# Kernel tuning notes

Measured on AMD Instinct MI355X. Metric: run time of the kernel, lower is better.

## Reference

```python
import jax, jax.numpy as jnp
import numpy as np

B, L, D, H, FFN = 4, 1024, 1024, 16, 4096
DPH = D // H
EPS = 1e-5

def layer_norm(x, g, b):
    mu = jnp.mean(x, axis=-1, keepdims=True)
    var = jnp.mean(jnp.square(x - mu), axis=-1, keepdims=True)
    return (x - mu) * jax.lax.rsqrt(var + EPS) * g + b

def setup_inputs() -> dict:
    key = jax.random.key(0)
    ks = jax.random.split(key, 12)
    s = 0.02
    return {
        "inputs": jax.random.normal(ks[0], (B, L, D), dtype=jnp.float32),
        "Wq": jax.random.normal(ks[1], (D, D), dtype=jnp.float32) * s,
        "bq": jnp.zeros((D,), jnp.float32),
        "Wk": jax.random.normal(ks[2], (D, D), dtype=jnp.float32) * s,
        "bk": jnp.zeros((D,), jnp.float32),
        "Wv": jax.random.normal(ks[3], (D, D), dtype=jnp.float32) * s,
        "bv": jnp.zeros((D,), jnp.float32),
        "Wo": jax.random.normal(ks[4], (D, D), dtype=jnp.float32) * s,
        "bo": jnp.zeros((D,), jnp.float32),
        "ln1_g": jnp.ones((D,), jnp.float32),
        "ln1_b": jnp.zeros((D,), jnp.float32),
        "W1": jax.random.normal(ks[5], (D, FFN), dtype=jnp.float32) * s,  # conv1d k=1 == linear
        "b1": jnp.zeros((FFN,), jnp.float32),
        "W2": jax.random.normal(ks[6], (FFN, D), dtype=jnp.float32) * s,
        "b2": jnp.zeros((D,), jnp.float32),
        "ln2_g": jnp.ones((D,), jnp.float32),
        "ln2_b": jnp.zeros((D,), jnp.float32),
    }

def reference(inputs, Wq, bq, Wk, bk, Wv, bv, Wo, bo, ln1_g, ln1_b,
              W1, b1, W2, b2, ln2_g, ln2_b):
    residual = inputs
    # QKV projections, then the original's raw view(B*H, L, DPH) split (NOT a transpose split)
    q = (inputs @ Wq + bq).reshape(B * H, L, DPH)
    k = (inputs @ Wk + bk).reshape(B * H, L, DPH)
    v = (inputs @ Wv + bv).reshape(B * H, L, DPH)
    scale = DPH ** -0.5
    scores = jnp.einsum('bqd,bkd->bqk', q, k) * scale  # [B*H, L, L]
    attention = jax.nn.softmax(scores, axis=-1)
    context = jnp.einsum('bqk,bkd->bqd', attention, v).reshape(B, L, D)
    out = context @ Wo + bo
    out = layer_norm(residual + out, ln1_g, ln1_b)
    # Positionwise FFN: two 1x1 conv1d == two linears with relu
    ffn = jax.nn.relu(out @ W1 + b1) @ W2 + b2
    out = layer_norm(out + ffn, ln2_g, ln2_b)
    return out, attention
```

## Files before the change

kernel.cpp:

```cpp
#include <hip/hip_runtime.h>
#include <hip/hip_bf16.h>
#include <stdint.h>


using bf16_t  = __hip_bfloat16;
using short8  = __attribute__((ext_vector_type(8))) short;
using short4v = __attribute__((ext_vector_type(4))) short;
using f32x4   = __attribute__((ext_vector_type(4))) float;

#define DEV static __device__ __forceinline__

DEV short bfbits(float f) {
  bf16_t h = __float2bfloat16(f);
  union { bf16_t h; short s; } u; u.h = h; return u.s;
}

__global__ __launch_bounds__(256) void k_f32_to_bf16(const float* __restrict__ in,
                                                     bf16_t* __restrict__ out) {
  size_t i = ((size_t)blockIdx.x * 256 + threadIdx.x) * 4;
  f32x4 x = *(const f32x4*)(in + i);
  short4v o;
  o[0] = bfbits(x[0]); o[1] = bfbits(x[1]); o[2] = bfbits(x[2]); o[3] = bfbits(x[3]);
  *(short4v*)((short*)out + i) = o;
}

__global__ __launch_bounds__(256) void k_transpose_f32_bf16(const float* __restrict__ in,
                                                            bf16_t* __restrict__ out,
                                                            int R, int C) {
  __shared__ float tile[32][33];
  int tx = threadIdx.x & 31, ty = threadIdx.x >> 5;
  int r0 = blockIdx.y * 32, c0 = blockIdx.x * 32;
  #pragma unroll
  for (int i = 0; i < 4; ++i)
    tile[ty + i * 8][tx] = in[(size_t)(r0 + ty + i * 8) * C + c0 + tx];
  __syncthreads();
  #pragma unroll
  for (int i = 0; i < 4; ++i)
    out[(size_t)(c0 + ty + i * 8) * R + r0 + tx] = __float2bfloat16(tile[tx][ty + i * 8]);
}

__global__ __launch_bounds__(256) void k_transpose_bf16_b(const bf16_t* __restrict__ in,
                                                          bf16_t* __restrict__ out,
                                                          int R, int C, long sIn, long sOut) {
  __shared__ bf16_t tile[32][33];
  const bf16_t* inz = in + (size_t)blockIdx.z * sIn;
  bf16_t* outz = out + (size_t)blockIdx.z * sOut;
  int tx = threadIdx.x & 31, ty = threadIdx.x >> 5;
  int r0 = blockIdx.y * 32, c0 = blockIdx.x * 32;
  #pragma unroll
  for (int i = 0; i < 4; ++i)
    tile[ty + i * 8][tx] = inz[(size_t)(r0 + ty + i * 8) * C + c0 + tx];
  __syncthreads();
  #pragma unroll
  for (int i = 0; i < 4; ++i)
    outz[(size_t)(c0 + ty + i * 8) * R + r0 + tx] = tile[tx][ty + i * 8];
}

template<int BM, int BN, bool AF32, bool ALPHA, bool BIAS, bool RELU, bool RESID,
         bool OUTF, bool OUTB>
__global__ __launch_bounds__(256)
void k_gemm_bt(const void* __restrict__ Ap, const bf16_t* __restrict__ Btp,
               float* __restrict__ Cf, bf16_t* __restrict__ Cb,
               const float* __restrict__ bias, const float* __restrict__ resid,
               int Kdim, int lda, int ldb, int ldc, float alpha,
               long strA, long strB, long strC) {
  constexpr int BK = 32, LDSK = 40;
  constexpr int WTM = BM / 2, WTN = BN / 2;
  constexpr int MI = WTM / 16, NI = WTN / 16;
  __shared__ __align__(16) bf16_t sA[BM][LDSK];
  __shared__ __align__(16) bf16_t sB[BN][LDSK];

  const int tid = threadIdx.x;
  const int lane = tid & 63;
  const int wv = tid >> 6;
  const int wm = wv & 1, wn = wv >> 1;
  const int z = blockIdx.z;
  const size_t m0 = (size_t)blockIdx.y * BM;
  const size_t n0 = (size_t)blockIdx.x * BN;

  const bf16_t* A16 = AF32 ? nullptr : ((const bf16_t*)Ap + (size_t)z * strA);
  const float*  A32 = AF32 ? ((const float*)Ap + (size_t)z * strA) : nullptr;
  const bf16_t* Bp  = Btp + (size_t)z * strB;

  f32x4 acc[MI][NI] = {};

  const int srow = tid >> 2;
  const int skc  = (tid & 3) * 8;

  for (int k0 = 0; k0 < Kdim; k0 += BK) {
    #pragma unroll
    for (int j = 0; j < BM / 64; ++j) {
      int r = j * 64 + srow;
      if (AF32) {
        const float* p = A32 + (m0 + r) * (size_t)lda + k0 + skc;
        f32x4 f0 = *(const f32x4*)p;
        f32x4 f1 = *(const f32x4*)(p + 4);
        short8 v;
        v[0] = bfbits(f0[0]); v[1] = bfbits(f0[1]); v[2] = bfbits(f0[2]); v[3] = bfbits(f0[3]);
        v[4] = bfbits(f1[0]); v[5] = bfbits(f1[1]); v[6] = bfbits(f1[2]); v[7] = bfbits(f1[3]);
        *(short8*)(&sA[r][skc]) = v;
      } else {
        *(short8*)(&sA[r][skc]) =
            *(const short8*)(A16 + (m0 + r) * (size_t)lda + k0 + skc);
      }
    }
    #pragma unroll
    for (int j = 0; j < BN / 64; ++j) {
      int r = j * 64 + srow;
      *(short8*)(&sB[r][skc]) =
          *(const short8*)(Bp + (n0 + r) * (size_t)ldb + k0 + skc);
    }
    __syncthreads();

    const int fm = wm * WTM + (lane & 15);
    const int fn = wn * WTN + (lane & 15);
    const int fk = (lane >> 4) * 8;
    short8 av[MI], bvv[NI];
    #pragma unroll
    for (int mi = 0; mi < MI; ++mi) av[mi] = *(const short8*)(&sA[fm + mi * 16][fk]);
    #pragma unroll
    for (int ni = 0; ni < NI; ++ni) bvv[ni] = *(const short8*)(&sB[fn + ni * 16][fk]);
    #pragma unroll
    for (int mi = 0; mi < MI; ++mi)
      #pragma unroll
      for (int ni = 0; ni < NI; ++ni)
        acc[mi][ni] = __builtin_amdgcn_mfma_f32_16x16x32_bf16(av[mi], bvv[ni],
                                                              acc[mi][ni], 0, 0, 0);
    __syncthreads();
  }

  const size_t cz = (size_t)z * strC;
  const int col0 = (int)n0 + wn * WTN + (lane & 15);
  const int row0 = (int)m0 + wm * WTM + ((lane >> 4) << 2);
  #pragma unroll
  for (int ni = 0; ni < NI; ++ni) {
    const int col = col0 + ni * 16;
    const float bval = BIAS ? bias[col] : 0.0f;
    #pragma unroll
    for (int mi = 0; mi < MI; ++mi) {
      #pragma unroll
      for (int r = 0; r < 4; ++r) {
        int row = row0 + mi * 16 + r;
        float v = acc[mi][ni][r];
        if (ALPHA) v *= alpha;
        v += bval;
        size_t off = cz + (size_t)row * ldc + col;
        if (RESID) v += resid[off];
        if (RELU) v = fmaxf(v, 0.0f);
        if (OUTF) Cf[off] = v;
        if (OUTB) Cb[off] = __float2bfloat16(v);
      }
    }
  }
}

__global__ __launch_bounds__(256) void k_flash_attn(const bf16_t* __restrict__ Qb,
                                                    const bf16_t* __restrict__ Kb,
                                                    const bf16_t* __restrict__ Vt,
                                                    float* __restrict__ attn,
                                                    bf16_t* __restrict__ ctx) {
  constexpr int LP = 72;
  __shared__ __align__(16) bf16_t sQ[128][LP];
  __shared__ __align__(16) bf16_t sK[64][LP];
  __shared__ __align__(16) bf16_t sP[128][LP];
  __shared__ __align__(16) bf16_t sV[64][LP];

  const int tid = threadIdx.x;
  const int lane = tid & 63;
  const int wv = tid >> 6;
  const int z = blockIdx.y;
  const int m0 = blockIdx.x * 128;

  const bf16_t* Qz = Qb + (size_t)z * 65536;
  const bf16_t* Kz = Kb + (size_t)z * 65536;
  const bf16_t* Vz = Vt + (size_t)z * 65536;
  float* az = attn + (size_t)z * 1048576;
  bf16_t* cz = ctx + (size_t)z * 65536;

  #pragma unroll
  for (int j = 0; j < 4; ++j) {
    int ii = j * 256 + tid;
    int r = ii >> 3, c = (ii & 7) * 8;
    *(short8*)(&sQ[r][c]) = *(const short8*)(Qz + (size_t)(m0 + r) * 64 + c);
  }
  __syncthreads();

  const int fr = lane & 15;
  const int fk = (lane >> 4) * 8;
  const int crow = (lane >> 4) << 2;

  short8 qf[2][2];
  #pragma unroll
  for (int mi = 0; mi < 2; ++mi)
    #pragma unroll
    for (int ks = 0; ks < 2; ++ks)
      qf[mi][ks] = *(const short8*)(&sQ[wv * 32 + mi * 16 + fr][ks * 32 + fk]);

  float m_run[2][4], s_run[2][4];
  #pragma unroll
  for (int mi = 0; mi < 2; ++mi)
    #pragma unroll
    for (int r = 0; r < 4; ++r) { m_run[mi][r] = -1e30f; s_run[mi][r] = 0.0f; }

  for (int c0 = 0; c0 < 1024; c0 += 64) {
    #pragma unroll
    for (int j = 0; j < 2; ++j) {
      int ii = j * 256 + tid;
      int r = ii >> 3, c = (ii & 7) * 8;
      *(short8*)(&sK[r][c]) = *(const short8*)(Kz + (size_t)(c0 + r) * 64 + c);
    }
    __syncthreads();
    f32x4 acc[2][4] = {};
    #pragma unroll
    for (int ks = 0; ks < 2; ++ks) {
      short8 bf[4];
      #pragma unroll
      for (int ni = 0; ni < 4; ++ni)
        bf[ni] = *(const short8*)(&sK[ni * 16 + fr][ks * 32 + fk]);
      #pragma unroll
      for (int mi = 0; mi < 2; ++mi)
        #pragma unroll
        for (int ni = 0; ni < 4; ++ni)
          acc[mi][ni] = __builtin_amdgcn_mfma_f32_16x16x32_bf16(qf[mi][ks], bf[ni],
                                                                acc[mi][ni], 0, 0, 0);
    }
    __syncthreads();
    #pragma unroll
    for (int mi = 0; mi < 2; ++mi)
      #pragma unroll
      for (int r = 0; r < 4; ++r) {
        float mx = fmaxf(fmaxf(acc[0][0][r], acc[0][0][r]), acc[mi][0][r]);
        mx = acc[mi][0][r];
        #pragma unroll
        for (int ni = 1; ni < 4; ++ni) mx = fmaxf(mx, acc[mi][ni][r]);
        mx *= 0.125f;
        #pragma unroll
        for (int o = 1; o < 16; o <<= 1) mx = fmaxf(mx, __shfl_xor(mx, o, 64));
        float mn = fmaxf(m_run[mi][r], mx);
        float se = 0.0f;
        #pragma unroll
        for (int ni = 0; ni < 4; ++ni) se += __expf(acc[mi][ni][r] * 0.125f - mn);
        #pragma unroll
        for (int o = 1; o < 16; o <<= 1) se += __shfl_xor(se, o, 64);
        s_run[mi][r] = s_run[mi][r] * __expf(m_run[mi][r] - mn) + se;
        m_run[mi][r] = mn;
      }
  }

  float inv_s[2][4];
  #pragma unroll
  for (int mi = 0; mi < 2; ++mi)
    #pragma unroll
    for (int r = 0; r < 4; ++r) inv_s[mi][r] = 1.0f / s_run[mi][r];

  f32x4 cacc[2][4] = {};
  for (int c0 = 0; c0 < 1024; c0 += 64) {
    #pragma unroll
    for (int j = 0; j < 2; ++j) {
      int ii = j * 256 + tid;
      int r = ii >> 3, c = (ii & 7) * 8;
      *(short8*)(&sK[r][c]) = *(const short8*)(Kz + (size_t)(c0 + r) * 64 + c);
      *(short8*)(&sV[r][c]) = *(const short8*)(Vz + (size_t)r * 1024 + c0 + c);
    }
    __syncthreads();
    f32x4 acc[2][4] = {};
    #pragma unroll
    for (int ks = 0; ks < 2; ++ks) {
      short8 bf[4];
      #pragma unroll
      for (int ni = 0; ni < 4; ++ni)
        bf[ni] = *(const short8*)(&sK[ni * 16 + fr][ks * 32 + fk]);
      #pragma unroll
      for (int mi = 0; mi < 2; ++mi)
        #pragma unroll
        for (int ni = 0; ni < 4; ++ni)
          acc[mi][ni] = __builtin_amdgcn_mfma_f32_16x16x32_bf16(qf[mi][ks], bf[ni],
                                                                acc[mi][ni], 0, 0, 0);
    }
    #pragma unroll
    for (int mi = 0; mi < 2; ++mi)
      #pragma unroll
      for (int ni = 0; ni < 4; ++ni)
        #pragma unroll
        for (int r = 0; r < 4; ++r) {
          int row = wv * 32 + mi * 16 + crow + r;
          float p = __expf(acc[mi][ni][r] * 0.125f - m_run[mi][r]) * inv_s[mi][r];
          az[(size_t)(m0 + row) * 1024 + c0 + ni * 16 + fr] = p;
          sP[row][ni * 16 + fr] = __float2bfloat16(p);
        }
    __syncthreads();
    #pragma unroll
    for (int ks = 0; ks < 2; ++ks) {
      short8 pa[2], vb[4];
      #pragma unroll
      for (int mi = 0; mi < 2; ++mi)
        pa[mi] = *(const short8*)(&sP[wv * 32 + mi * 16 + fr][ks * 32 + fk]);
      #pragma unroll
      for (int ni = 0; ni < 4; ++ni)
        vb[ni] = *(const short8*)(&sV[ni * 16 + fr][ks * 32 + fk]);
      #pragma unroll
      for (int mi = 0; mi < 2; ++mi)
        #pragma unroll
        for (int ni = 0; ni < 4; ++ni)
          cacc[mi][ni] = __builtin_amdgcn_mfma_f32_16x16x32_bf16(pa[mi], vb[ni],
                                                                 cacc[mi][ni], 0, 0, 0);
    }
    __syncthreads();
  }

  #pragma unroll
  for (int mi = 0; mi < 2; ++mi)
    #pragma unroll
    for (int ni = 0; ni < 4; ++ni)
      #pragma unroll
      for (int r = 0; r < 4; ++r) {
        int row = wv * 32 + mi * 16 + crow + r;
        cz[(size_t)(m0 + row) * 64 + ni * 16 + fr] = __float2bfloat16(cacc[mi][ni][r]);
      }
}

__global__ __launch_bounds__(256) void k_layernorm(float* __restrict__ io,
                                                   bf16_t* __restrict__ ob,
                                                   const float* __restrict__ g,
                                                   const float* __restrict__ bta) {
  float* r = io + (size_t)blockIdx.x * 1024;
  const int t = threadIdx.x;
  f32x4 x = *(const f32x4*)(r + t * 4);
  float s = x[0] + x[1] + x[2] + x[3];
  float s2 = x[0] * x[0] + x[1] * x[1] + x[2] * x[2] + x[3] * x[3];
  #pragma unroll
  for (int o = 32; o > 0; o >>= 1) { s += __shfl_xor(s, o, 64); s2 += __shfl_xor(s2, o, 64); }
  __shared__ float as[4], as2[4];
  if ((t & 63) == 0) { as[t >> 6] = s; as2[t >> 6] = s2; }
  __syncthreads();
  s = as[0] + as[1] + as[2] + as[3];
  s2 = as2[0] + as2[1] + as2[2] + as2[3];
  float mu = s * (1.0f / 1024.0f);
  float var = s2 * (1.0f / 1024.0f) - mu * mu;
  float rs = rsqrtf(var + 1e-5f);
  f32x4 gg = *(const f32x4*)(g + t * 4);
  f32x4 bb = *(const f32x4*)(bta + t * 4);
  f32x4 y;
  #pragma unroll
  for (int i = 0; i < 4; ++i) y[i] = (x[i] - mu) * rs * gg[i] + bb[i];
  *(f32x4*)(r + t * 4) = y;
  if (ob) {
    short4v o4;
    o4[0] = bfbits(y[0]); o4[1] = bfbits(y[1]); o4[2] = bfbits(y[2]); o4[3] = bfbits(y[3]);
    *(short4v*)((short*)ob + (size_t)blockIdx.x * 1024 + t * 4) = o4;
  }
}

extern "C" void kernel_launch(void* const* d_in, const int* in_sizes, int n_in,
                              void* d_out, int out_size, void* d_ws, size_t ws_size,
                              hipStream_t stream) {
  (void)in_sizes; (void)n_in; (void)out_size;
  const float* inputs = (const float*)d_in[0];
  const float* Wq = (const float*)d_in[1];  const float* bq = (const float*)d_in[2];
  const float* Wk = (const float*)d_in[3];  const float* bk = (const float*)d_in[4];
  const float* Wv = (const float*)d_in[5];  const float* bv = (const float*)d_in[6];
  const float* Wo = (const float*)d_in[7];  const float* bo = (const float*)d_in[8];
  const float* ln1g = (const float*)d_in[9];  const float* ln1b = (const float*)d_in[10];
  const float* W1 = (const float*)d_in[11]; const float* b1 = (const float*)d_in[12];
  const float* W2 = (const float*)d_in[13]; const float* b2 = (const float*)d_in[14];
  const float* ln2g = (const float*)d_in[15]; const float* ln2b = (const float*)d_in[16];

  const size_t MB = 1ull << 20;
  if (ws_size < 96 * MB) return;

  char* ws = (char*)d_ws;
  bf16_t* WQT  = (bf16_t*)(ws + 0 * MB);
  bf16_t* WKT  = (bf16_t*)(ws + 2 * MB);
  bf16_t* WVT  = (bf16_t*)(ws + 4 * MB);
  bf16_t* WOT  = (bf16_t*)(ws + 6 * MB);
  bf16_t* W1T  = (bf16_t*)(ws + 8 * MB);
  bf16_t* W2T  = (bf16_t*)(ws + 16 * MB);
  bf16_t* XB   = (bf16_t*)(ws + 24 * MB);
  bf16_t* QB   = (bf16_t*)(ws + 32 * MB);
  bf16_t* KB   = (bf16_t*)(ws + 40 * MB);
  bf16_t* VB   = (bf16_t*)(ws + 48 * MB);
  bf16_t* VT   = (bf16_t*)(ws + 56 * MB);
  bf16_t* CTX  = (bf16_t*)(ws + 24 * MB);
  float*  OUT1F = (float*)(ws + 40 * MB);
  bf16_t* OUT1B = (bf16_t*)(ws + 32 * MB);
  bf16_t* HB   = (bf16_t*)(ws + 64 * MB);

  float* outF = (float*)d_out;
  float* attn = outF + 4194304;

  k_f32_to_bf16<<<4096, 256, 0, stream>>>(inputs, XB);
  k_transpose_f32_bf16<<<dim3(32, 32), 256, 0, stream>>>(Wq, WQT, 1024, 1024);
  k_transpose_f32_bf16<<<dim3(32, 32), 256, 0, stream>>>(Wk, WKT, 1024, 1024);
  k_transpose_f32_bf16<<<dim3(32, 32), 256, 0, stream>>>(Wv, WVT, 1024, 1024);
  k_transpose_f32_bf16<<<dim3(32, 32), 256, 0, stream>>>(Wo, WOT, 1024, 1024);
  k_transpose_f32_bf16<<<dim3(128, 32), 256, 0, stream>>>(W1, W1T, 1024, 4096);
  k_transpose_f32_bf16<<<dim3(32, 128), 256, 0, stream>>>(W2, W2T, 4096, 1024);

  k_gemm_bt<128, 128, false, false, true, false, false, false, true>
      <<<dim3(8, 32, 1), 256, 0, stream>>>(XB, WQT, nullptr, QB, bq, nullptr,
                                           1024, 1024, 1024, 1024, 1.0f, 0, 0, 0);
  k_gemm_bt<128, 128, false, false, true, false, false, false, true>
      <<<dim3(8, 32, 1), 256, 0, stream>>>(XB, WKT, nullptr, KB, bk, nullptr,
                                           1024, 1024, 1024, 1024, 1.0f, 0, 0, 0);
  k_gemm_bt<128, 128, false, false, true, false, false, false, true>
      <<<dim3(8, 32, 1), 256, 0, stream>>>(XB, WVT, nullptr, VB, bv, nullptr,
                                           1024, 1024, 1024, 1024, 1.0f, 0, 0, 0);

  k_transpose_bf16_b<<<dim3(2, 32, 64), 256, 0, stream>>>(VB, VT, 1024, 64, 65536, 65536);

  k_flash_attn<<<dim3(8, 64), 256, 0, stream>>>(QB, KB, VT, attn, CTX);

  k_gemm_bt<128, 128, false, false, true, false, true, true, false>
      <<<dim3(8, 32, 1), 256, 0, stream>>>(CTX, WOT, OUT1F, nullptr, bo, inputs,
                                           1024, 1024, 1024, 1024, 1.0f, 0, 0, 0);

  k_layernorm<<<4096, 256, 0, stream>>>(OUT1F, OUT1B, ln1g, ln1b);

  k_gemm_bt<128, 128, false, false, true, true, false, false, true>
      <<<dim3(32, 32, 1), 256, 0, stream>>>(OUT1B, W1T, nullptr, HB, b1, nullptr,
                                            1024, 1024, 1024, 4096, 1.0f, 0, 0, 0);

  k_gemm_bt<128, 128, false, false, true, false, true, true, false>
      <<<dim3(8, 32, 1), 256, 0, stream>>>(HB, W2T, outF, nullptr, b2, OUT1F,
                                           4096, 4096, 4096, 1024, 1.0f, 0, 0, 0);

  k_layernorm<<<4096, 256, 0, stream>>>(outF, nullptr, ln2g, ln2b);
}
```

Before: 762.2 us.

## Use direct global-to-LDS loads in GEMM and fuse QKV projections into one launch

The GEMM now stages A and B tiles with global_load_lds (16-byte direct-to-LDS loads), which skips the register round trip, and drops the padded LDS layout for a dense 32-wide row layout. The three Q/K/V projections run as one launch over a 3072-wide output, relying on WQT/WKT/WVT being contiguous in the workspace, and pick the bias and output buffer per 1024-column slice. The unpadded LDS layout may cause bank conflicts on the fragment reads. The change also removes a redundant max computation in attention.

After: 707.7 us. -7.2%, faster.

```diff
diff --git a/kernel.cpp b/kernel.cpp
--- a/kernel.cpp
+++ b/kernel.cpp
@@ -13,6 +13,12 @@
 DEV short bfbits(float f) {
   bf16_t h = __float2bfloat16(f);
   union { bf16_t h; short s; } u; u.h = h; return u.s;
+}
+
+DEV void gload_lds16(const bf16_t* g, bf16_t* lds) {
+  __builtin_amdgcn_global_load_lds(
+      (const __attribute__((address_space(1))) void*)g,
+      (__attribute__((address_space(3))) void*)lds, 16, 0, 0);
 }
 
 __global__ __launch_bounds__(256) void k_f32_to_bf16(const float* __restrict__ in,
@@ -56,70 +62,55 @@
     outz[(size_t)(c0 + ty + i * 8) * R + r0 + tx] = tile[tx][ty + i * 8];
 }
 
-template<int BM, int BN, bool AF32, bool ALPHA, bool BIAS, bool RELU, bool RESID,
-         bool OUTF, bool OUTB>
+template<int BM, int BN, bool ALPHA, bool BIAS, bool RELU, bool RESID,
+         bool OUTF, bool OUTB, bool QKV3>
 __global__ __launch_bounds__(256)
-void k_gemm_bt(const void* __restrict__ Ap, const bf16_t* __restrict__ Btp,
+void k_gemm_bt(const bf16_t* __restrict__ A, const bf16_t* __restrict__ Bt,
                float* __restrict__ Cf, bf16_t* __restrict__ Cb,
-               const float* __restrict__ bias, const float* __restrict__ resid,
-               int Kdim, int lda, int ldb, int ldc, float alpha,
-               long strA, long strB, long strC) {
-  constexpr int BK = 32, LDSK = 40;
+               const float* __restrict__ bias, const float* __restrict__ bias2,
+               const float* __restrict__ bias3, const float* __restrict__ resid,
+               int Kdim, int lda, int ldb, int ldc, float alpha) {
+  constexpr int BK = 32;
   constexpr int WTM = BM / 2, WTN = BN / 2;
   constexpr int MI = WTM / 16, NI = WTN / 16;
-  __shared__ __align__(16) bf16_t sA[BM][LDSK];
-  __shared__ __align__(16) bf16_t sB[BN][LDSK];
+  __shared__ __align__(16) bf16_t sA[BM * BK];
+  __shared__ __align__(16) bf16_t sB[BN * BK];
 
   const int tid = threadIdx.x;
   const int lane = tid & 63;
   const int wv = tid >> 6;
   const int wm = wv & 1, wn = wv >> 1;
-  const int z = blockIdx.z;
   const size_t m0 = (size_t)blockIdx.y * BM;
   const size_t n0 = (size_t)blockIdx.x * BN;
 
-  const bf16_t* A16 = AF32 ? nullptr : ((const bf16_t*)Ap + (size_t)z * strA);
-  const float*  A32 = AF32 ? ((const float*)Ap + (size_t)z * strA) : nullptr;
-  const bf16_t* Bp  = Btp + (size_t)z * strB;
-
   f32x4 acc[MI][NI] = {};
 
-  const int srow = tid >> 2;
-  const int skc  = (tid & 3) * 8;
+  const int rr = lane >> 2, cc = (lane & 3) * 8;
+  const bf16_t* Arow = A + (m0 + rr) * (size_t)lda + cc;
+  const bf16_t* Brow = Bt + (n0 + rr) * (size_t)ldb + cc;
+
+  const int fm = wm * WTM + (lane & 15);
+  const int fn = wn * WTN + (lane & 15);
+  const int fk = (lane >> 4) * 8;
 
   for (int k0 = 0; k0 < Kdim; k0 += BK) {
     #pragma unroll
     for (int j = 0; j < BM / 64; ++j) {
-      int r = j * 64 + srow;
-      if (AF32) {
-        const float* p = A32 + (m0 + r) * (size_t)lda + k0 + skc;
-        f32x4 f0 = *(const f32x4*)p;
-        f32x4 f1 = *(const f32x4*)(p + 4);
-        short8 v;
-        v[0] = bfbits(f0[0]); v[1] = bfbits(f0[1]); v[2] = bfbits(f0[2]); v[3] = bfbits(f0[3]);
-        v[4] = bfbits(f1[0]); v[5] = bfbits(f1[1]); v[6] = bfbits(f1[2]); v[7] = bfbits(f1[3]);
-        *(short8*)(&sA[r][skc]) = v;
-      } else {
-        *(short8*)(&sA[r][skc]) =
-            *(const short8*)(A16 + (m0 + r) * (size_t)lda + k0 + skc);
-      }
+      int c = j * 4 + wv;
+      gload_lds16(Arow + (size_t)c * 16 * lda + k0, sA + c * 512);
     }
     #pragma unroll
     for (int j = 0; j < BN / 64; ++j) {
-      int r = j * 64 + srow;
-      *(short8*)(&sB[r][skc]) =
-          *(const short8*)(Bp + (n0 + r) * (size_t)ldb + k0 + skc);
-    }
-    __syncthreads();
-
-    const int fm = wm * WTM + (lane & 15);
-    const int fn = wn * WTN + (lane & 15);
-    const int fk = (lane >> 4) * 8;
+      int c = j * 4 + wv;
+      gload_lds16(Brow + (size_t)c * 16 * ldb + k0, sB + c * 512);
+    }
+    __syncthreads();
+
     short8 av[MI], bvv[NI];
     #pragma unroll
-    for (int mi = 0; mi < MI; ++mi) av[mi] = *(const short8*)(&sA[fm + mi * 16][fk]);
-    #pragma unroll
-    for (int ni = 0; ni < NI; ++ni) bvv[ni] = *(const short8*)(&sB[fn + ni * 16][fk]);
+    for (int mi = 0; mi < MI; ++mi) av[mi] = *(const short8*)(sA + (fm + mi * 16) * BK + fk);
+    #pragma unroll
+    for (int ni = 0; ni < NI; ++ni) bvv[ni] = *(const short8*)(sB + (fn + ni * 16) * BK + fk);
     #pragma unroll
     for (int mi = 0; mi < MI; ++mi)
       #pragma unroll
@@ -129,13 +120,17 @@
     __syncthreads();
   }
 
-  const size_t cz = (size_t)z * strC;
+  const int tz = QKV3 ? (int)(n0 >> 10) : 0;
+  const float* bp = BIAS ? (QKV3 ? (tz == 0 ? bias : (tz == 1 ? bias2 : bias3))
+                                 : bias) : nullptr;
+  bf16_t* cb = QKV3 ? (Cb + (size_t)tz * 4194304) : Cb;
   const int col0 = (int)n0 + wn * WTN + (lane & 15);
   const int row0 = (int)m0 + wm * WTM + ((lane >> 4) << 2);
   #pragma unroll
   for (int ni = 0; ni < NI; ++ni) {
     const int col = col0 + ni * 16;
-    const float bval = BIAS ? bias[col] : 0.0f;
+    const int colw = QKV3 ? (col & 1023) : col;
+    const float bval = BIAS ? bp[colw] : 0.0f;
     #pragma unroll
     for (int mi = 0; mi < MI; ++mi) {
       #pragma unroll
@@ -144,11 +139,11 @@
         float v = acc[mi][ni][r];
         if (ALPHA) v *= alpha;
         v += bval;
-        size_t off = cz + (size_t)row * ldc + col;
+        size_t off = (size_t)row * ldc + colw;
         if (RESID) v += resid[off];
         if (RELU) v = fmaxf(v, 0.0f);
         if (OUTF) Cf[off] = v;
-        if (OUTB) Cb[off] = __float2bfloat16(v);
+        if (OUTB) cb[off] = __float2bfloat16(v);
       }
     }
   }
@@ -229,8 +224,7 @@
     for (int mi = 0; mi < 2; ++mi)
       #pragma unroll
       for (int r = 0; r < 4; ++r) {
-        float mx = fmaxf(fmaxf(acc[0][0][r], acc[0][0][r]), acc[mi][0][r]);
-        mx = acc[mi][0][r];
+        float mx = acc[mi][0][r];
         #pragma unroll
         for (int ni = 1; ni < 4; ++ni) mx = fmaxf(mx, acc[mi][ni][r]);
         mx *= 0.125f;
@@ -377,9 +371,9 @@
   bf16_t* W2T  = (bf16_t*)(ws + 16 * MB);
   bf16_t* XB   = (bf16_t*)(ws + 24 * MB);
   bf16_t* QB   = (bf16_t*)(ws + 32 * MB);
-  bf16_t* KB   = (bf16_t*)(ws + 40 * MB);
   bf16_t* VB   = (bf16_t*)(ws + 48 * MB);
   bf16_t* VT   = (bf16_t*)(ws + 56 * MB);
+  bf16_t* KB   = (bf16_t*)(ws + 40 * MB);
   bf16_t* CTX  = (bf16_t*)(ws + 24 * MB);
   float*  OUT1F = (float*)(ws + 40 * MB);
   bf16_t* OUT1B = (bf16_t*)(ws + 32 * MB);
@@ -396,33 +390,27 @@
   k_transpose_f32_bf16<<<dim3(128, 32), 256, 0, stream>>>(W1, W1T, 1024, 4096);
   k_transpose_f32_bf16<<<dim3(32, 128), 256, 0, stream>>>(W2, W2T, 4096, 1024);
 
-  k_gemm_bt<128, 128, false, false, true, false, false, false, true>
-      <<<dim3(8, 32, 1), 256, 0, stream>>>(XB, WQT, nullptr, QB, bq, nullptr,
-                                           1024, 1024, 1024, 1024, 1.0f, 0, 0, 0);
-  k_gemm_bt<128, 128, false, false, true, false, false, false, true>
-      <<<dim3(8, 32, 1), 256, 0, stream>>>(XB, WKT, nullptr, KB, bk, nullptr,
-                                           1024, 1024, 1024, 1024, 1.0f, 0, 0, 0);
-  k_gemm_bt<128, 128, false, false, true, false, false, false, true>
-      <<<dim3(8, 32, 1), 256, 0, stream>>>(XB, WVT, nullptr, VB, bv, nullptr,
-                                           1024, 1024, 1024, 1024, 1.0f, 0, 0, 0);
+  k_gemm_bt<128, 128, false, true, false, false, false, true, true>
+      <<<dim3(24, 32), 256, 0, stream>>>(XB, WQT, nullptr, QB, bq, bk, bv, nullptr,
+                                         1024, 1024, 1024, 1024, 1.0f);
 
   k_transpose_bf16_b<<<dim3(2, 32, 64), 256, 0, stream>>>(VB, VT, 1024, 64, 65536, 65536);
 
   k_flash_attn<<<dim3(8, 64), 256, 0, stream>>>(QB, KB, VT, attn, CTX);
 
-  k_gemm_bt<128, 128, false, false, true, false, true, true, false>
-      <<<dim3(8, 32, 1), 256, 0, stream>>>(CTX, WOT, OUT1F, nullptr, bo, inputs,
-                                           1024, 1024, 1024, 1024, 1.0f, 0, 0, 0);
+  k_gemm_bt<128, 128, false, true, false, true, true, false, false>
+      <<<dim3(8, 32), 256, 0, stream>>>(CTX, WOT, OUT1F, nullptr, bo, nullptr, nullptr,
+                                        inputs, 1024, 1024, 1024, 1024, 1.0f);
 
   k_layernorm<<<4096, 256, 0, stream>>>(OUT1F, OUT1B, ln1g, ln1b);
 
-  k_gemm_bt<128, 128, false, false, true, true, false, false, true>
-      <<<dim3(32, 32, 1), 256, 0, stream>>>(OUT1B, W1T, nullptr, HB, b1, nullptr,
-                                            1024, 1024, 1024, 4096, 1.0f, 0, 0, 0);
-
-  k_gemm_bt<128, 128, false, false, true, false, true, true, false>
-      <<<dim3(8, 32, 1), 256, 0, stream>>>(HB, W2T, outF, nullptr, b2, OUT1F,
-                                           4096, 4096, 4096, 1024, 1.0f, 0, 0, 0);
+  k_gemm_bt<128, 128, false, true, true, false, false, true, false>
+      <<<dim3(32, 32), 256, 0, stream>>>(OUT1B, W1T, nullptr, HB, b1, nullptr, nullptr,
+                                         nullptr, 1024, 1024, 1024, 4096, 1.0f);
+
+  k_gemm_bt<128, 128, false, true, false, true, true, false, false>
+      <<<dim3(8, 32), 256, 0, stream>>>(HB, W2T, outF, nullptr, b2, nullptr, nullptr,
+                                        OUT1F, 4096, 4096, 4096, 1024, 1.0f);
 
   k_layernorm<<<4096, 256, 0, stream>>>(outF, nullptr, ln2g, ln2b);
 }
```
